# Performance work log

Measured on AMD Instinct MI355X. Metric: run time of the kernel, lower is better.

Reference implementation:

```python
import jax, jax.numpy as jnp
import numpy as np

W, B, S, D = 4, 1, 1024, 1024   # simulated world_size, batch, local seq, embed_dim
H, DS, HM = 16, 64, 4            # num_heads, summary_dim, meta_heads


def mha(q, k, v, w_in, b_in, w_out, b_out, nheads):
    """torch nn.MultiheadAttention (batch_first). Returns (out, head-averaged weights)."""
    d = q.shape[-1]
    hd = d // nheads
    wq, wk, wv = jnp.split(w_in, 3, axis=0)
    bq, bk, bv = jnp.split(b_in, 3)
    Bq, Sq, _ = q.shape
    Sk = k.shape[1]
    qh = (q @ wq.T + bq).reshape(Bq, Sq, nheads, hd)
    kh = (k @ wk.T + bk).reshape(Bq, Sk, nheads, hd)
    vh = (v @ wv.T + bv).reshape(Bq, Sk, nheads, hd)
    scores = jnp.einsum('bqhd,bkhd->bhqk', qh, kh) / float(np.sqrt(hd))
    attn = jax.nn.softmax(scores, axis=-1)
    out = jnp.einsum('bhqk,bkhd->bqhd', attn, vh).reshape(Bq, Sq, d)
    return out @ w_out.T + b_out, attn.mean(axis=1)


def attn_stats(attn):
    """attn: (B, S) -> (B, 4) [entropy, gini, max, top5]."""
    ent = -(attn * jnp.log(attn + 1e-8)).sum(-1, keepdims=True)
    s = jnp.sort(attn, axis=-1)
    n = attn.shape[-1]
    idx = jnp.arange(1, n + 1, dtype=attn.dtype)
    gini = 2.0 * (idx * s).sum(-1) / (n * s.sum(-1) + 1e-8) - (n + 1) / n
    mx = attn.max(-1, keepdims=True)
    k = min(5, n)
    top5 = jax.lax.top_k(attn, k)[0].sum(-1, keepdims=True)
    return jnp.concatenate([ent, gini[..., None], mx, top5], axis=-1)


def _forward(x, local_in_w, local_in_b, local_out_w, local_out_b,
             sum_query, sum_in_w, sum_in_b, sum_out_w, sum_out_b,
             pat_w1, pat_b1, pat_w2, pat_b2, comb_w, comb_b,
             meta_in_w, meta_in_b, meta_out_w, meta_out_b,
             route_w1, route_b1, route_w2, route_b2,
             cross_in_w, cross_in_b, cross_out_w, cross_out_b,
             gate_w, gate_b, proj_w, proj_b):
    nW = x.shape[0]

    # 1) local attention per rank: (W,B,S,D)
    local = jax.vmap(lambda xc: mha(xc, xc, xc, local_in_w, local_in_b,
                                    local_out_w, local_out_b, H)[0])(x)

    # 2) chunk summary per rank
    def summarize(lo):
        q = jnp.broadcast_to(sum_query, (lo.shape[0], 1, lo.shape[-1]))
        content, w = mha(q, lo, lo, sum_in_w, sum_in_b, sum_out_w, sum_out_b, H)
        content, w = content[:, 0], w[:, 0]              # (B,D), (B,S)
        pat = attn_stats(w)                               # (B,4)
        pat = jax.nn.relu(pat @ pat_w1.T + pat_b1) @ pat_w2.T + pat_b2
        return jnp.concatenate([content, pat], axis=-1) @ comb_w.T + comb_b

    summaries = jax.vmap(summarize)(local)                # (W,B,DS)
    all_sum = jnp.transpose(summaries, (1, 0, 2))         # (B,W,DS) = all-gather

    # 3) meta attention over chunk summaries -> routing weights
    refined, chunk_attn = mha(all_sum, all_sum, all_sum,
                              meta_in_w, meta_in_b, meta_out_w, meta_out_b, HM)
    logits = (jax.nn.relu(refined @ route_w1.T + route_b1) @ route_w2.T + route_b2)[..., 0]
    routing = jax.nn.softmax(logits, axis=-1)             # (B,W)

    all_chunks = jnp.transpose(local, (1, 0, 2, 3))       # (B,W,S,D) = all-gather

    # 4) selective cross-attention + gated combine, per rank
    def per_rank(r, lo):
        rm = routing * (1.0 - jax.nn.one_hot(r, nW, dtype=routing.dtype))
        rm = rm / (rm.sum(-1, keepdims=True) + 1e-8)
        kv = jnp.einsum('bw,bwsd->bsd', rm, all_chunks)
        cross, _ = mha(lo, kv, kv, cross_in_w, cross_in_b, cross_out_w, cross_out_b, H)
        g = jax.nn.sigmoid(jnp.concatenate([lo, cross], axis=-1) @ gate_w.T + gate_b)
        comb = g * cross + (1.0 - g) * lo
        return comb @ proj_w.T + proj_b

    out = jax.vmap(per_rank)(jnp.arange(nW), local)       # (W,B,S,D)
    return out


def setup_inputs() -> dict:
    key = jax.random.key(0)
    ks = iter(jax.random.split(key, 40))
    p = lambda *shape: jax.random.normal(next(ks), shape, dtype=jnp.float32) * 0.02
    inp = {
        'x': jax.random.normal(next(ks), (W, B, S, D), dtype=jnp.float32),
        'local_in_w': p(3 * D, D), 'local_in_b': p(3 * D),
        'local_out_w': p(D, D), 'local_out_b': p(D),
        'sum_query': p(1, 1, D),
        'sum_in_w': p(3 * D, D), 'sum_in_b': p(3 * D),
        'sum_out_w': p(D, D), 'sum_out_b': p(D),
        'pat_w1': p(DS, 4), 'pat_b1': p(DS),
        'pat_w2': p(DS, DS), 'pat_b2': p(DS),
        'comb_w': p(DS, D + DS), 'comb_b': p(DS),
        'meta_in_w': p(3 * DS, DS), 'meta_in_b': p(3 * DS),
        'meta_out_w': p(DS, DS), 'meta_out_b': p(DS),
        'route_w1': p(DS, DS), 'route_b1': p(DS),
        'route_w2': p(1, DS), 'route_b2': p(1),
        'cross_in_w': p(3 * D, D), 'cross_in_b': p(3 * D),
        'cross_out_w': p(D, D), 'cross_out_b': p(D),
        'gate_w': p(D, 2 * D), 'gate_b': p(D),
        'proj_w': p(D, D), 'proj_b': p(D),
    }
    return inp


def reference(x, local_in_w, local_in_b, local_out_w, local_out_b,
              sum_query, sum_in_w, sum_in_b, sum_out_w, sum_out_b,
              pat_w1, pat_b1, pat_w2, pat_b2, comb_w, comb_b,
              meta_in_w, meta_in_b, meta_out_w, meta_out_b,
              route_w1, route_b1, route_w2, route_b2,
              cross_in_w, cross_in_b, cross_out_w, cross_out_b,
              gate_w, gate_b, proj_w, proj_b):
    return _forward(x, local_in_w, local_in_b, local_out_w, local_out_b,
                    sum_query, sum_in_w, sum_in_b, sum_out_w, sum_out_b,
                    pat_w1, pat_b1, pat_w2, pat_b2, comb_w, comb_b,
                    meta_in_w, meta_in_b, meta_out_w, meta_out_b,
                    route_w1, route_b1, route_w2, route_b2,
                    cross_in_w, cross_in_b, cross_out_w, cross_out_b,
                    gate_w, gate_b, proj_w, proj_b)
```

## Files before the change

### kernel.cpp

```cpp
#include <hip/hip_runtime.h>
#include <hip/hip_bf16.h>
#include <stdint.h>

typedef uint16_t u16;
typedef __attribute__((ext_vector_type(8))) short short8;
typedef __attribute__((ext_vector_type(4))) short short4v;
typedef __attribute__((ext_vector_type(8))) unsigned short ushort8;
typedef __attribute__((ext_vector_type(4))) float f32x4;

#define AS1 __attribute__((address_space(1)))
#define AS3 __attribute__((address_space(3)))

__device__ __forceinline__ float b2f(u16 u){
  union{uint32_t i; float f;} v; v.i=((uint32_t)u)<<16; return v.f;
}
__device__ __forceinline__ u16 f2b(float f){
  union{uint32_t i; float f;} v; v.f=f;
  return (u16)((v.i + 0x7fffu + ((v.i>>16)&1u))>>16);
}
__device__ __forceinline__ u16 f2bf(float f){
  __hip_bfloat16 h = __float2bfloat16(f);
  return *reinterpret_cast<u16*>(&h);
}

struct CvtP { const float* src[8]; u16* dst[8]; long n[8]; };
__global__ void cvt_multi(CvtP p) {
  const int seg = blockIdx.y;
  const long i = ((long)blockIdx.x*256 + threadIdx.x)*8;
  if (i >= p.n[seg]) return;
  const float* in = p.src[seg];
  float4 a = *(const float4*)&in[i];
  float4 b = *(const float4*)&in[i+4];
  ushort8 o;
  o[0]=f2b(a.x); o[1]=f2b(a.y); o[2]=f2b(a.z); o[3]=f2b(a.w);
  o[4]=f2b(b.x); o[5]=f2b(b.y); o[6]=f2b(b.z); o[7]=f2b(b.w);
  *(ushort8*)&p.dst[seg][i] = o;
}

struct GemmP {
  const u16* A; const u16* B; u16* C; const float* bias;
  const u16* B2; u16* C2; const float* bias2;
  const u16* A2; const u16* lr; const u16* cr;
  long lda, ldb, ldc, ldb2, ldc2;
  int K, Nstore, Nstore2, ySplit, act, outf;
  float scale;
};

template<int BM>
__global__ __launch_bounds__(512) void gemm_nt(GemmP p) {
  constexpr int MI = BM / 32;
  __shared__ __align__(16) u16 lA[2][BM*32];
  __shared__ __align__(16) u16 lB[2][4096];
  const int t = threadIdx.x;
  const int wave = t >> 6, lane = t & 63;
  int by = blockIdx.y;
  const u16* Bp; u16* Cp; const float* bias; long ldb, ldc; int nst;
  if (by >= p.ySplit) {
    by -= p.ySplit; Bp = p.B2; Cp = p.C2; bias = p.bias2;
    ldb = p.ldb2; ldc = p.ldc2; nst = p.Nstore2;
  } else {
    Bp = p.B; Cp = p.C; bias = p.bias; ldb = p.ldb; ldc = p.ldc; nst = p.Nstore;
  }
  const u16* B = Bp + (long)by * 128 * ldb;
  const int srow = t >> 2, skk = (t & 3) * 8;
  const int wr = wave >> 2, wc = wave & 3;
  const int fr = lane & 15, fk = (lane >> 4) * 8;
  f32x4 acc[MI][2] = {};

  const int stepsPerSeg = p.K >> 5;
  const int nseg = p.A2 ? 2 : 1;
  const int total = nseg * stepsPerSeg;
  const u16* A0p = p.A + (long)blockIdx.x * BM * p.lda;
  const u16* A1p = p.A2 ? (p.A2 + (long)blockIdx.x * BM * p.lda) : A0p;

  auto stage = [&](int s, int b) {
    const int sg = (s >= stepsPerSeg) ? 1 : 0;
    const int k0 = (s - sg*stepsPerSeg) << 5;
    const u16* Ax = sg ? A1p : A0p;
    const u16* Bx = B + (long)sg * p.K;
    if (t < BM*4)
      __builtin_amdgcn_global_load_lds((const AS1 void*)(Ax + (long)srow*p.lda + k0 + skk),
                                       (AS3 void*)&lA[b][t*8], 16, 0, 0);
    __builtin_amdgcn_global_load_lds((const AS1 void*)(Bx + (long)srow*ldb + k0 + skk),
                                     (AS3 void*)&lB[b][t*8], 16, 0, 0);
  };

  stage(0, 0);
  __syncthreads();
  int cur = 0;
  for (int s = 0; s < total; ++s) {
    if (s + 1 < total) stage(s + 1, cur ^ 1);
    short8 av[MI], bv[2];
    #pragma unroll
    for (int mi = 0; mi < MI; ++mi) av[mi] = *(const short8*)&lA[cur][(wr*(BM/2) + mi*16 + fr)*32 + fk];
    #pragma unroll
    for (int ni = 0; ni < 2; ++ni) bv[ni] = *(const short8*)&lB[cur][(wc*32 + ni*16 + fr)*32 + fk];
    #pragma unroll
    for (int mi = 0; mi < MI; ++mi)
      #pragma unroll
      for (int ni = 0; ni < 2; ++ni)
        acc[mi][ni] = __builtin_amdgcn_mfma_f32_16x16x32_bf16(av[mi], bv[ni], acc[mi][ni], 0, 0, 0);
    __syncthreads();
    cur ^= 1;
  }

  const int rbase = blockIdx.x*BM + wr*(BM/2);
  const int cbase = by*128 + wc*32;
  const int rsub = (lane >> 4) * 4;
  #pragma unroll
  for (int ni = 0; ni < 2; ++ni) {
    const int col = cbase + ni*16 + fr;
    if (col >= nst) continue;
    const float bs = bias ? bias[col] : 0.f;
    #pragma unroll
    for (int mi = 0; mi < MI; ++mi) {
      #pragma unroll
      for (int j = 0; j < 4; ++j) {
        float v = acc[mi][ni][j] * p.scale + bs;
        const long idx = (long)(rbase + mi*16 + rsub + j) * ldc + col;
        if (p.act == 2) {
          const float gv = 1.f / (1.f + __expf(-v));
          const float cv = b2f(p.cr[idx]);
          const float lv = b2f(p.lr[idx]);
          Cp[idx] = f2b(gv*cv + (1.f - gv)*lv);
        } else {
          if (p.act == 1) v = 1.f / (1.f + __expf(-v));
          if (p.outf) ((float*)Cp)[idx] = v;
          else        Cp[idx] = f2b(v);
        }
      }
    }
  }
}

struct FlashP {
  const u16 *q, *k, *v; u16* o;
  long ldq, ldkv, ldo;
  long qB, kvB, oB;
};

__global__ __launch_bounds__(256) void flash_k(FlashP p) {
  const int t = threadIdx.x, w4 = t >> 6, lane = t & 63;
  const int bid = blockIdx.x;
  const int qt = bid >> 6;
  const int h  = bid & 15;
  const int wz = (bid >> 4) & 3;
  const int fr = lane & 15, g = lane >> 4, fk = g * 8;
  __shared__ __align__(16) u16 kt[64][72];
  __shared__ __align__(16) u16 vt[64][72];
  __shared__ __align__(16) u16 pl[4][32][72];

  const u16* Q = p.q + (long)wz*p.qB + (long)(qt*128 + w4*32)*p.ldq + h*64;
  const u16* K = p.k + (long)wz*p.kvB + h*64;
  const u16* V = p.v + (long)wz*p.kvB + h*64;

  short8 aq[2][2];
  #pragma unroll
  for (int f = 0; f < 2; ++f) {
    aq[f][0] = *(const short8*)&Q[(long)(f*16 + fr)*p.ldq + fk];
    aq[f][1] = *(const short8*)&Q[(long)(f*16 + fr)*p.ldq + 32 + fk];
  }

  f32x4 acc[2][4] = {};
  float ml[2] = {-3e38f, -3e38f}, ll[2] = {0.f, 0.f};
  const float C = 0.125f * 1.44269504f;

  const int krow = t >> 2, kseg = (t & 3) * 16;
  const int vp = t & 31, vc = (t >> 5) * 8;

  short8 kr0, kr1, vr0, vr1;
  kr0 = *(const short8*)&K[(long)krow*p.ldkv + kseg];
  kr1 = *(const short8*)&K[(long)krow*p.ldkv + kseg + 8];
  vr0 = *(const short8*)&V[(long)(2*vp)*p.ldkv + vc];
  vr1 = *(const short8*)&V[(long)(2*vp + 1)*p.ldkv + vc];

  for (int it = 0; it < 16; ++it) {
    *(short8*)&kt[krow][kseg]     = kr0;
    *(short8*)&kt[krow][kseg + 8] = kr1;
    #pragma unroll
    for (int e = 0; e < 8; ++e) {
      const uint32_t pk = (uint32_t)(uint16_t)vr0[e] | ((uint32_t)(uint16_t)vr1[e] << 16);
      *(uint32_t*)&vt[vc + e][2*vp] = pk;
    }
    __syncthreads();

    if (it + 1 < 16) {
      const int kn = (it + 1) * 64;
      kr0 = *(const short8*)&K[(long)(kn + krow)*p.ldkv + kseg];
      kr1 = *(const short8*)&K[(long)(kn + krow)*p.ldkv + kseg + 8];
      vr0 = *(const short8*)&V[(long)(kn + 2*vp)*p.ldkv + vc];
      vr1 = *(const short8*)&V[(long)(kn + 2*vp + 1)*p.ldkv + vc];
    }

    f32x4 s[2][4] = {};
    __builtin_amdgcn_s_setprio(1);
    #pragma unroll
    for (int ni = 0; ni < 4; ++ni) {
      short8 bk0 = *(const short8*)&kt[ni*16 + fr][fk];
      short8 bk1 = *(const short8*)&kt[ni*16 + fr][32 + fk];
      #pragma unroll
      for (int f = 0; f < 2; ++f) {
        s[f][ni] = __builtin_amdgcn_mfma_f32_16x16x32_bf16(bk0, aq[f][0], s[f][ni], 0, 0, 0);
        s[f][ni] = __builtin_amdgcn_mfma_f32_16x16x32_bf16(bk1, aq[f][1], s[f][ni], 0, 0, 0);
      }
    }
    __builtin_amdgcn_s_setprio(0);

    #pragma unroll
    for (int f = 0; f < 2; ++f) {
      float rm = s[f][0][0];
      #pragma unroll
      for (int ni = 0; ni < 4; ++ni)
        #pragma unroll
        for (int j = 0; j < 4; ++j) rm = fmaxf(rm, s[f][ni][j]);
      rm = fmaxf(rm, __shfl_xor(rm, 16, 64));
      rm = fmaxf(rm, __shfl_xor(rm, 32, 64));
      const float rml = rm * C;

      if (__any(rml > ml[f] + 11.5f)) {
        const float mnl = fmaxf(ml[f], rml);
        const float al = exp2f(ml[f] - mnl);
        const float a0 = __shfl(al, g*4 + 0, 64);
        const float a1 = __shfl(al, g*4 + 1, 64);
        const float a2 = __shfl(al, g*4 + 2, 64);
        const float a3 = __shfl(al, g*4 + 3, 64);
        #pragma unroll
        for (int nv = 0; nv < 4; ++nv) {
          acc[f][nv][0] *= a0; acc[f][nv][1] *= a1;
          acc[f][nv][2] *= a2; acc[f][nv][3] *= a3;
        }
        ll[f] *= al;
        ml[f] = mnl;
      }

      float rs = 0.f;
      u16 pb[4][4];
      #pragma unroll
      for (int ni = 0; ni < 4; ++ni)
        #pragma unroll
        for (int j = 0; j < 4; ++j) {
          const float pv = exp2f(s[f][ni][j]*C - ml[f]);
          rs += pv;
          pb[ni][j] = f2bf(pv);
        }
      rs += __shfl_xor(rs, 16, 64);
      rs += __shfl_xor(rs, 32, 64);
      ll[f] += rs;

      #pragma unroll
      for (int ni = 0; ni < 4; ++ni) {
        short4v pk4;
        pk4[0] = (short)pb[ni][0]; pk4[1] = (short)pb[ni][1];
        pk4[2] = (short)pb[ni][2]; pk4[3] = (short)pb[ni][3];
        *(short4v*)&pl[w4][f*16 + fr][ni*16 + g*4] = pk4;
      }
    }

    __builtin_amdgcn_s_setprio(1);
    #pragma unroll
    for (int ks = 0; ks < 2; ++ks) {
      short8 pa0 = *(const short8*)&pl[w4][fr][ks*32 + fk];
      short8 pa1 = *(const short8*)&pl[w4][16 + fr][ks*32 + fk];
      #pragma unroll
      for (int nv = 0; nv < 4; ++nv) {
        short8 bvv = *(const short8*)&vt[nv*16 + fr][ks*32 + fk];
        acc[0][nv] = __builtin_amdgcn_mfma_f32_16x16x32_bf16(pa0, bvv, acc[0][nv], 0, 0, 0);
        acc[1][nv] = __builtin_amdgcn_mfma_f32_16x16x32_bf16(pa1, bvv, acc[1][nv], 0, 0, 0);
      }
    }
    __builtin_amdgcn_s_setprio(0);
    __syncthreads();
  }

  u16* O = p.o + (long)wz*p.oB + (long)(qt*128 + w4*32)*p.ldo + h*64;
  #pragma unroll
  for (int f = 0; f < 2; ++f) {
    const float l0 = __shfl(ll[f], g*4 + 0, 64);
    const float l1 = __shfl(ll[f], g*4 + 1, 64);
    const float l2 = __shfl(ll[f], g*4 + 2, 64);
    const float l3 = __shfl(ll[f], g*4 + 3, 64);
    const float inv[4] = {1.f/l0, 1.f/l1, 1.f/l2, 1.f/l3};
    #pragma unroll
    for (int j = 0; j < 4; ++j)
      #pragma unroll
      for (int nv = 0; nv < 4; ++nv)
        O[(long)(f*16 + g*4 + j)*p.ldo + nv*16 + fr] = f2bf(acc[f][nv][j] * inv[j]);
  }
}

__global__ void gemv_qs(const float* sq, const float* w, const float* b, float* out) {
  const int t = threadIdx.x, nl = t & 63, kq = t >> 6;
  const int n = blockIdx.x*64 + nl;
  const float* row = w + (long)n * 1024 + kq*256;
  const float* q = sq + kq*256;
  float s = 0.f;
  for (int k = 0; k < 256; k += 4) {
    float4 ww = *(const float4*)&row[k];
    float4 qq = *(const float4*)&q[k];
    s += qq.x*ww.x + qq.y*ww.y + qq.z*ww.z + qq.w*ww.w;
  }
  __shared__ float ps[4][64];
  ps[kq][nl] = s;
  __syncthreads();
  if (t < 64) out[blockIdx.x*64 + t] = ps[0][t]+ps[1][t]+ps[2][t]+ps[3][t] + b[blockIdx.x*64 + t];
}

__global__ void sum_attend(const float* qs, const u16* sumkv, float* content, float* pall) {
  const int h = blockIdx.x, w = blockIdx.y, t = threadIdx.x;
  const int lane = t & 63, wv = t >> 6;
  __shared__ float qsh[64];
  __shared__ float sc[1024];
  __shared__ float rmax[4], rsum[4];
  __shared__ float po[4][64];
  if (t < 64) qsh[t] = qs[h*64 + t];
  __syncthreads();
  const u16* kbase = sumkv + (long)w*2097152 + h*64;
  float e[4];
  float mx = -1e30f;
  #pragma unroll
  for (int j = 0; j < 4; ++j) {
    const int k = j*256 + t;
    const u16* krow = kbase + (long)k * 2048;
    float s = 0.f;
    #pragma unroll
    for (int d = 0; d < 64; d += 8) {
      ushort8 kk = *(const ushort8*)&krow[d];
      #pragma unroll
      for (int q = 0; q < 8; ++q) s += qsh[d+q] * b2f(kk[q]);
    }
    s *= 0.125f;
    e[j] = s;
    mx = fmaxf(mx, s);
  }
  #pragma unroll
  for (int o = 32; o; o >>= 1) mx = fmaxf(mx, __shfl_xor(mx, o, 64));
  if (lane == 0) rmax[wv] = mx;
  __syncthreads();
  mx = fmaxf(fmaxf(rmax[0],rmax[1]), fmaxf(rmax[2],rmax[3]));
  float sum = 0.f;
  #pragma unroll
  for (int j = 0; j < 4; ++j) { e[j] = __expf(e[j]-mx); sum += e[j]; }
  #pragma unroll
  for (int o = 32; o; o >>= 1) sum += __shfl_xor(sum, o, 64);
  if (lane == 0) rsum[wv] = sum;
  __syncthreads();
  const float inv = 1.f / (rsum[0]+rsum[1]+rsum[2]+rsum[3]);
  float* pr = pall + ((long)w*16 + h)*1024;
  #pragma unroll
  for (int j = 0; j < 4; ++j) {
    const int k = j*256 + t;
    const float pn = e[j]*inv;
    sc[k] = pn;
    pr[k] = pn;
  }
  __syncthreads();
  const u16* vbase = sumkv + (long)w*2097152 + 1024 + h*64;
  float o = 0.f;
  const int k0 = wv*256;
  for (int k = k0; k < k0+256; ++k) o += sc[k] * b2f(vbase[(long)k*2048 + lane]);
  po[wv][lane] = o;
  __syncthreads();
  if (t < 64) content[(long)w*1024 + h*64 + t] = po[0][t]+po[1][t]+po[2][t]+po[3][t];
}

__global__ void wavg_k(const float* pall, float* wavg) {
  const int w = blockIdx.y, k = blockIdx.x*256 + threadIdx.x;
  float s = 0.f;
  #pragma unroll
  for (int h = 0; h < 16; ++h) s += pall[((long)w*16 + h)*1024 + k];
  wavg[w*1024 + k] = s * (1.f/16.f);
}

__global__ void contproj_k(const float* content, const float* w_, const float* b, float* out) {
  const int w = blockIdx.y, t = threadIdx.x;
  const int nl = t & 63, kq = t >> 6;
  const int n = blockIdx.x*64 + nl;
  const float* c = content + w*1024 + kq*256;
  const float* row = w_ + (long)n * 1024 + kq*256;
  float s = 0.f;
  for (int k = 0; k < 256; k += 4) {
    float4 ww = *(const float4*)&row[k];
    s += c[k]*ww.x + c[k+1]*ww.y + c[k+2]*ww.z + c[k+3]*ww.w;
  }
  __shared__ float ps[4][64];
  ps[kq][nl] = s;
  __syncthreads();
  if (t < 64) out[w*1024 + blockIdx.x*64 + t] = ps[0][t]+ps[1][t]+ps[2][t]+ps[3][t] + b[blockIdx.x*64 + t];
}

__global__ void stats1_k(const float* wavg, float* part) {
  const int c = blockIdx.x, w = blockIdx.y, t = threadIdx.x;
  __shared__ float a[1024];
  for (int i = t; i < 1024; i += 256) a[i] = wavg[w*1024 + i];
  __syncthreads();
  const int jl = t & 63, iq = t >> 6;
  const int j = c*64 + jl;
  const float aj = a[j];
  int pr = 0;
  const int i0 = iq*256;
  #pragma unroll 8
  for (int i = i0; i < i0+256; ++i) {
    const float ai = a[i];
    pr += (ai < aj) || (ai == aj && i < j);
  }
  __shared__ int prs[4][64];
  prs[iq][jl] = pr;
  __syncthreads();
  if (t < 64) {
    const int rank = 1 + prs[0][jl] + prs[1][jl] + prs[2][jl] + prs[3][jl];
    float ent = -aj * logf(aj + 1e-8f);
    float gnum = (float)rank * aj;
    float ssum = aj;
    float mx = aj;
    float top5 = (rank >= 1020) ? aj : 0.f;
    #pragma unroll
    for (int o = 32; o; o >>= 1) {
      ent += __shfl_xor(ent, o, 64);
      gnum += __shfl_xor(gnum, o, 64);
      ssum += __shfl_xor(ssum, o, 64);
      mx = fmaxf(mx, __shfl_xor(mx, o, 64));
      top5 += __shfl_xor(top5, o, 64);
    }
    if (t == 0) {
      float* pp = part + ((w*16 + c) * 5);
      pp[0]=ent; pp[1]=gnum; pp[2]=ssum; pp[3]=mx; pp[4]=top5;
    }
  }
}

__global__ void stats2_k(const float* part, float* stats) {
  const int w = blockIdx.x, t = threadIdx.x;
  const int c = t & 15, stat = t >> 4;
  float v = 0.f;
  const bool active = stat < 5;
  if (active) v = part[(w*16 + c)*5 + stat];
  #pragma unroll
  for (int o = 8; o; o >>= 1) {
    const float ov = __shfl_xor(v, o, 64);
    v = (stat == 3) ? fmaxf(v, ov) : (v + ov);
  }
  __shared__ float r5[5];
  if (active && c == 0) r5[stat] = v;
  __syncthreads();
  if (t == 0) {
    stats[w*4+0] = r5[0];
    stats[w*4+1] = 2.f*r5[1]/(1024.f*r5[2] + 1e-8f) - 1025.f/1024.f;
    stats[w*4+2] = r5[3];
    stats[w*4+3] = r5[4];
  }
}

__global__ void patsum_k(const float* stats, const float* contprj,
                         const float* pw1, const float* pb1, const float* pw2, const float* pb2,
                         const float* combw, const float* combb, float* summ) {
  const int w = blockIdx.x, t = threadIdx.x;
  const int nl = t & 63, kq = t >> 6;
  __shared__ float p1[64], pat[64];
  __shared__ float ps[4][64];
  __shared__ float ps2[4][64];
  if (t < 64) {
    float s = 0.f;
    #pragma unroll
    for (int k = 0; k < 4; ++k) s += stats[w*4+k] * pw1[t*4+k];
    p1[t] = fmaxf(s + pb1[t], 0.f);
  }
  __syncthreads();
  {
    float s = 0.f;
    const float* rw = pw2 + (long)nl*64 + kq*16;
    const float* pp = p1 + kq*16;
    #pragma unroll
    for (int k = 0; k < 16; ++k) s += pp[k] * rw[k];
    ps[kq][nl] = s;
  }
  __syncthreads();
  if (t < 64) pat[t] = ps[0][t]+ps[1][t]+ps[2][t]+ps[3][t] + pb2[t];
  __syncthreads();
  const float* c = contprj + w*1024;
  const float* row = combw + (long)nl * 1088;
  float s = 0.f;
  const int k0 = kq*272;
  for (int k = k0; k < k0+272; ++k) {
    const float rv = row[k];
    const float cv = (k < 1024) ? c[k] : pat[k-1024];
    s += cv * rv;
  }
  ps2[kq][nl] = s;
  __syncthreads();
  if (t < 64) summ[w*64 + t] = ps2[0][t]+ps2[1][t]+ps2[2][t]+ps2[3][t] + combb[t];
}

__global__ void meta_k(const float* summ, const float* miw, const float* mib,
                       const float* mow, const float* mob, const float* rw1, const float* rb1,
                       const float* rw2, const float* rb2, float* routing) {
  const int t = threadIdx.x;
  __shared__ float qkv[4][192];
  __shared__ float sc[64];
  __shared__ float o[4][64];
  __shared__ float rf[4][64];
  __shared__ float t1[4][64];
  __shared__ float lg[4];
  for (int idx = t; idx < 768; idx += 64) {
    const int w = idx / 192, rrow = idx % 192;
    const float* rw = miw + (long)rrow * 64;
    float s = 0.f;
    for (int k = 0; k < 64; ++k) s += summ[w*64+k] * rw[k];
    qkv[w][rrow] = s + mib[rrow];
  }
  __syncthreads();
  {
    const int h = t >> 4, i = (t >> 2) & 3, j = t & 3;
    float s = 0.f;
    #pragma unroll
    for (int d = 0; d < 16; ++d) s += qkv[i][h*16+d] * qkv[j][64 + h*16+d];
    sc[t] = s * 0.25f;
  }
  __syncthreads();
  if (t < 16) {
    const float a0=sc[t*4], a1=sc[t*4+1], a2=sc[t*4+2], a3=sc[t*4+3];
    const float m = fmaxf(fmaxf(a0,a1), fmaxf(a2,a3));
    const float e0=__expf(a0-m), e1=__expf(a1-m), e2=__expf(a2-m), e3=__expf(a3-m);
    const float s = e0+e1+e2+e3;
    sc[t*4]=e0/s; sc[t*4+1]=e1/s; sc[t*4+2]=e2/s; sc[t*4+3]=e3/s;
  }
  __syncthreads();
  for (int idx = t; idx < 256; idx += 64) {
    const int i = idx >> 6, c = idx & 63, h = c >> 4;
    float s = 0.f;
    #pragma unroll
    for (int j = 0; j < 4; ++j) s += sc[(h*4+i)*4+j] * qkv[j][128 + c];
    o[i][c] = s;
  }
  __syncthreads();
  for (int idx = t; idx < 256; idx += 64) {
    const int i = idx >> 6, n = idx & 63;
    const float* rw = mow + (long)n * 64;
    float s = 0.f;
    for (int k = 0; k < 64; ++k) s += o[i][k] * rw[k];
    rf[i][n] = s + mob[n];
  }
  __syncthreads();
  for (int idx = t; idx < 256; idx += 64) {
    const int i = idx >> 6, n = idx & 63;
    const float* rw = rw1 + (long)n * 64;
    float s = 0.f;
    for (int k = 0; k < 64; ++k) s += rf[i][k] * rw[k];
    t1[i][n] = fmaxf(s + rb1[n], 0.f);
  }
  __syncthreads();
  if (t < 4) {
    float s = 0.f;
    for (int k = 0; k < 64; ++k) s += t1[t][k] * rw2[k];
    lg[t] = s + rb2[0];
  }
  __syncthreads();
  if (t == 0) {
    const float m = fmaxf(fmaxf(lg[0],lg[1]), fmaxf(lg[2],lg[3]));
    float e[4], s = 0.f;
    #pragma unroll
    for (int i = 0; i < 4; ++i) { e[i] = __expf(lg[i]-m); s += e[i]; }
    #pragma unroll
    for (int i = 0; i < 4; ++i) routing[i] = e[i]/s;
  }
}

__global__ void kvr_k(const u16* local, const float* routing, u16* kvr) {
  const int r = blockIdx.y;
  const long e = ((long)blockIdx.x*256 + threadIdx.x) * 8;
  float rm[4]; float s = 0.f;
  #pragma unroll
  for (int w = 0; w < 4; ++w) { rm[w] = (w == r) ? 0.f : routing[w]; s += rm[w]; }
  const float inv = 1.f / (s + 1e-8f);
  ushort8 a0 = *(const ushort8*)&local[e];
  ushort8 a1 = *(const ushort8*)&local[1048576 + e];
  ushort8 a2 = *(const ushort8*)&local[2097152 + e];
  ushort8 a3 = *(const ushort8*)&local[3145728 + e];
  ushort8 out;
  #pragma unroll
  for (int j = 0; j < 8; ++j)
    out[j] = f2b((rm[0]*b2f(a0[j]) + rm[1]*b2f(a1[j]) + rm[2]*b2f(a2[j]) + rm[3]*b2f(a3[j])) * inv);
  *(ushort8*)&kvr[(long)r*1048576 + e] = out;
}

template<int BM>
static void gemmT(hipStream_t st, dim3 grid,
                  const u16* A, long lda, const u16* B, long ldb,
                  u16* C, long ldc, const float* bias,
                  int K, int N, float scale, int act, int outf) {
  GemmP p = {};
  p.A=A; p.B=B; p.C=C; p.bias=bias;
  p.lda=lda; p.ldb=ldb; p.ldc=ldc;
  p.K=K; p.Nstore=N; p.ySplit=1<<30; p.act=act; p.outf=outf; p.scale=scale;
  gemm_nt<BM><<<grid, dim3(512), 0, st>>>(p);
}

extern "C" void kernel_launch(void* const* d_in, const int* in_sizes, int n_in,
                              void* d_out, int out_size, void* d_ws, size_t ws_size,
                              hipStream_t stream) {
  (void)in_sizes; (void)n_in; (void)out_size; (void)ws_size;
  const float* x   = (const float*)d_in[0];
  const float* liw = (const float*)d_in[1];
  const float* lib = (const float*)d_in[2];
  const float* low = (const float*)d_in[3];
  const float* lob = (const float*)d_in[4];
  const float* sq  = (const float*)d_in[5];
  const float* siw = (const float*)d_in[6];
  const float* sib = (const float*)d_in[7];
  const float* sow = (const float*)d_in[8];
  const float* sob = (const float*)d_in[9];
  const float* pw1 = (const float*)d_in[10];
  const float* pb1 = (const float*)d_in[11];
  const float* pw2 = (const float*)d_in[12];
  const float* pb2 = (const float*)d_in[13];
  const float* cbw = (const float*)d_in[14];
  const float* cbb = (const float*)d_in[15];
  const float* miw = (const float*)d_in[16];
  const float* mib = (const float*)d_in[17];
  const float* mow = (const float*)d_in[18];
  const float* mob = (const float*)d_in[19];
  const float* rw1 = (const float*)d_in[20];
  const float* rb1 = (const float*)d_in[21];
  const float* rw2 = (const float*)d_in[22];
  const float* rb2 = (const float*)d_in[23];
  const float* ciw = (const float*)d_in[24];
  const float* cib = (const float*)d_in[25];
  const float* cow = (const float*)d_in[26];
  const float* cob = (const float*)d_in[27];
  const float* gw  = (const float*)d_in[28];
  const float* gb  = (const float*)d_in[29];
  const float* pw  = (const float*)d_in[30];
  const float* pb  = (const float*)d_in[31];

  char* ws = (char*)d_ws;
  u16* qkv    = (u16*)(ws + 0);
  u16* aout   = (u16*)(ws + 25165824);
  u16* local  = (u16*)(ws + 33554432);
  u16* scratch= (u16*)(ws + 41943040);
  u16* s2048  = (u16*)(ws + 79691776);
  u16* cq     = (u16*)(ws + 96468992);
  u16* kvr    = (u16*)(ws + 104857600);
  u16* crossb = (u16*)(ws + 113246208);
  char* sf = ws + 121634816;
  float* qs      = (float*)(sf + 0);
  float* pall    = (float*)(sf + 4096);
  float* wavg    = (float*)(sf + 266240);
  float* content = (float*)(sf + 282624);
  float* contprj = (float*)(sf + 299008);
  float* stats   = (float*)(sf + 315392);
  float* summ    = (float*)(sf + 315456);
  float* routing = (float*)(sf + 316480);
  float* part    = (float*)(sf + 316544);
  u16* siwkvb = (u16*)(ws + 122028032);
  u16* lowb   = (u16*)(ws + 126222336);
  u16* ciwb   = (u16*)(ws + 128319488);
  u16* cowb   = (u16*)(ws + 134610944);
  u16* gwb    = (u16*)(ws + 136708096);
  u16* pwb    = (u16*)(ws + 140902400);
  u16* xb   = crossb;
  u16* liwb = scratch;

  CvtP cp;
  cp.src[0]=x;   cp.dst[0]=xb;     cp.n[0]=4194304;
  cp.src[1]=liw; cp.dst[1]=liwb;   cp.n[1]=3145728;
  cp.src[2]=low; cp.dst[2]=lowb;   cp.n[2]=1048576;
  cp.src[3]=siw+1048576; cp.dst[3]=siwkvb; cp.n[3]=2097152;
  cp.src[4]=ciw; cp.dst[4]=ciwb;   cp.n[4]=3145728;
  cp.src[5]=cow; cp.dst[5]=cowb;   cp.n[5]=1048576;
  cp.src[6]=gw;  cp.dst[6]=gwb;    cp.n[6]=2097152;
  cp.src[7]=pw;  cp.dst[7]=pwb;    cp.n[7]=1048576;
  cvt_multi<<<dim3(2048, 8), dim3(256), 0, stream>>>(cp);

  gemmT<128>(stream, dim3(32,24), xb,1024, liwb,1024, qkv,3072, lib, 1024, 3072, 1.f, 0, 0);

  {
    FlashP fp;
    fp.q = qkv; fp.k = qkv + 1024; fp.v = qkv + 2048; fp.o = aout;
    fp.ldq = 3072; fp.ldkv = 3072; fp.ldo = 1024;
    fp.qB = 3145728; fp.kvB = 3145728; fp.oB = 1048576;
    flash_k<<<dim3(512), dim3(256), 0, stream>>>(fp);
  }

  gemmT<64>(stream, dim3(64,8), aout,1024, lowb,1024, local,1024, lob, 1024, 1024, 1.f, 0, 0);

  {
    GemmP p = {};
    p.A = local; p.lda = 1024; p.K = 1024; p.scale = 1.f;
    p.B = ciwb;   p.C = cq;    p.bias = cib;      p.ldb = 1024; p.ldc = 1024; p.Nstore = 1024;
    p.B2 = siwkvb; p.C2 = s2048; p.bias2 = sib+1024; p.ldb2 = 1024; p.ldc2 = 2048; p.Nstore2 = 2048;
    p.ySplit = 8;
    gemm_nt<128><<<dim3(32,24), dim3(512), 0, stream>>>(p);
  }

  gemv_qs<<<dim3(16), dim3(256), 0, stream>>>(sq, siw, sib, qs);
  sum_attend<<<dim3(16,4), dim3(256), 0, stream>>>(qs, s2048, content, pall);
  wavg_k<<<dim3(4,4), dim3(256), 0, stream>>>(pall, wavg);
  contproj_k<<<dim3(16,4), dim3(256), 0, stream>>>(content, sow, sob, contprj);
  stats1_k<<<dim3(16,4), dim3(256), 0, stream>>>(wavg, part);
  stats2_k<<<dim3(4), dim3(128), 0, stream>>>(part, stats);
  patsum_k<<<dim3(4), dim3(256), 0, stream>>>(stats, contprj, pw1, pb1, pw2, pb2, cbw, cbb, summ);

  meta_k<<<dim3(1), dim3(64), 0, stream>>>(summ, miw, mib, mow, mob, rw1, rb1, rw2, rb2, routing);

  kvr_k<<<dim3(512,4), dim3(256), 0, stream>>>(local, routing, kvr);

  gemmT<128>(stream, dim3(32,16), kvr,1024, ciwb+1048576,1024, s2048,2048, cib+1024, 1024, 2048, 1.f, 0, 0);

  {
    FlashP fp;
    fp.q = cq; fp.k = s2048; fp.v = s2048 + 1024; fp.o = aout;
    fp.ldq = 1024; fp.ldkv = 2048; fp.ldo = 1024;
    fp.qB = 1048576; fp.kvB = 2097152; fp.oB = 1048576;
    flash_k<<<dim3(512), dim3(256), 0, stream>>>(fp);
  }

  gemmT<64>(stream, dim3(64,8), aout,1024, cowb,1024, crossb,1024, cob, 1024, 1024, 1.f, 0, 0);

  {
    GemmP p = {};
    p.A = local; p.A2 = crossb; p.lr = local; p.cr = crossb;
    p.B = gwb; p.C = kvr; p.bias = gb;
    p.lda = 1024; p.ldb = 2048; p.ldc = 1024;
    p.K = 1024; p.Nstore = 1024; p.ySplit = 1<<30; p.act = 2; p.outf = 0; p.scale = 1.f;
    gemm_nt<64><<<dim3(64,8), dim3(512), 0, stream>>>(p);
  }

  gemmT<64>(stream, dim3(64,8), kvr,1024, pwb,1024, (u16*)d_out,1024, pb, 1024, 1024, 1.f, 0, 1);
}
```

Baseline: 425.5 us.

## Split flash attention over two KV halves and merge partials

Each flash attention launch now splits the key/value sequence into two halves, doubling the grid from 512 to 1024 blocks. Each half writes unnormalized fp32 partial outputs plus running max and sum to workspace. A new merge kernel rescales and combines the two partials into the bf16 output. The aim is better occupancy on a GPU with many CUs, at the cost of extra fp32 global traffic and one more launch per attention.

```diff
diff --git a/kernel.cpp b/kernel.cpp
--- a/kernel.cpp
+++ b/kernel.cpp
@@ -135,6 +135,7 @@
 
 struct FlashP {
   const u16 *q, *k, *v; u16* o;
+  float* pO; float* pml;
   long ldq, ldkv, ldo;
   long qB, kvB, oB;
 };
@@ -142,17 +143,19 @@
 __global__ __launch_bounds__(256) void flash_k(FlashP p) {
   const int t = threadIdx.x, w4 = t >> 6, lane = t & 63;
   const int bid = blockIdx.x;
-  const int qt = bid >> 6;
-  const int h  = bid & 15;
-  const int wz = (bid >> 4) & 3;
+  const int half = bid >> 9;
+  const int sub = bid & 511;
+  const int qt = sub >> 6;
+  const int h  = sub & 15;
+  const int wz = (sub >> 4) & 3;
   const int fr = lane & 15, g = lane >> 4, fk = g * 8;
   __shared__ __align__(16) u16 kt[64][72];
   __shared__ __align__(16) u16 vt[64][72];
   __shared__ __align__(16) u16 pl[4][32][72];
 
   const u16* Q = p.q + (long)wz*p.qB + (long)(qt*128 + w4*32)*p.ldq + h*64;
-  const u16* K = p.k + (long)wz*p.kvB + h*64;
-  const u16* V = p.v + (long)wz*p.kvB + h*64;
+  const u16* K = p.k + (long)wz*p.kvB + h*64 + (long)(half*512)*p.ldkv;
+  const u16* V = p.v + (long)wz*p.kvB + h*64 + (long)(half*512)*p.ldkv;
 
   short8 aq[2][2];
   #pragma unroll
@@ -174,7 +177,7 @@
   vr0 = *(const short8*)&V[(long)(2*vp)*p.ldkv + vc];
   vr1 = *(const short8*)&V[(long)(2*vp + 1)*p.ldkv + vc];
 
-  for (int it = 0; it < 16; ++it) {
+  for (int it = 0; it < 8; ++it) {
     *(short8*)&kt[krow][kseg]     = kr0;
     *(short8*)&kt[krow][kseg + 8] = kr1;
     #pragma unroll
@@ -184,7 +187,7 @@
     }
     __syncthreads();
 
-    if (it + 1 < 16) {
+    if (it + 1 < 8) {
       const int kn = (it + 1) * 64;
       kr0 = *(const short8*)&K[(long)(kn + krow)*p.ldkv + kseg];
       kr1 = *(const short8*)&K[(long)(kn + krow)*p.ldkv + kseg + 8];
@@ -272,19 +275,46 @@
     __syncthreads();
   }
 
-  u16* O = p.o + (long)wz*p.oB + (long)(qt*128 + w4*32)*p.ldo + h*64;
+  const long Rbase = ((long)(wz*16 + h))*1024 + qt*128 + w4*32;
+  float* PO  = p.pO  + (long)half*65536*64;
+  float* PML = p.pml + (long)half*65536*2;
   #pragma unroll
   for (int f = 0; f < 2; ++f) {
-    const float l0 = __shfl(ll[f], g*4 + 0, 64);
-    const float l1 = __shfl(ll[f], g*4 + 1, 64);
-    const float l2 = __shfl(ll[f], g*4 + 2, 64);
-    const float l3 = __shfl(ll[f], g*4 + 3, 64);
-    const float inv[4] = {1.f/l0, 1.f/l1, 1.f/l2, 1.f/l3};
     #pragma unroll
     for (int j = 0; j < 4; ++j)
       #pragma unroll
       for (int nv = 0; nv < 4; ++nv)
-        O[(long)(f*16 + g*4 + j)*p.ldo + nv*16 + fr] = f2bf(acc[f][nv][j] * inv[j]);
+        PO[(Rbase + f*16 + g*4 + j)*64 + nv*16 + fr] = acc[f][nv][j];
+    if (g == 0) {
+      PML[(Rbase + f*16 + fr)*2    ] = ml[f];
+      PML[(Rbase + f*16 + fr)*2 + 1] = ll[f];
+    }
+  }
+}
+
+__global__ __launch_bounds__(256) void fmerge_k(const float* pO, const float* pml, u16* out) {
+  const int t = threadIdx.x;
+  const long r = (long)blockIdx.x*64 + (t >> 2);
+  const int dq = (t & 3) * 16;
+  const float m0 = pml[r*2],            l0 = pml[r*2 + 1];
+  const float m1 = pml[131072 + r*2],   l1 = pml[131072 + r*2 + 1];
+  const float m  = fmaxf(m0, m1);
+  const float a0 = exp2f(m0 - m), a1 = exp2f(m1 - m);
+  const float inv = 1.f / (l0*a0 + l1*a1);
+  const float s0 = a0*inv, s1 = a1*inv;
+  const long  o0 = r*64 + dq;
+  const long  o1 = 4194304L + r*64 + dq;
+  const int wz = (int)(r >> 14), rem = (int)(r & 16383);
+  const int h = rem >> 10, qrow = rem & 1023;
+  u16* ob = out + (long)wz*1048576 + (long)qrow*1024 + h*64 + dq;
+  #pragma unroll
+  for (int dd = 0; dd < 4; ++dd) {
+    float4 v0 = *(const float4*)&pO[o0 + dd*4];
+    float4 v1 = *(const float4*)&pO[o1 + dd*4];
+    ob[dd*4 + 0] = f2bf(v0.x*s0 + v1.x*s1);
+    ob[dd*4 + 1] = f2bf(v0.y*s0 + v1.y*s1);
+    ob[dd*4 + 2] = f2bf(v0.z*s0 + v1.z*s1);
+    ob[dd*4 + 3] = f2bf(v0.w*s0 + v1.w*s1);
   }
 }
 
@@ -658,6 +688,8 @@
   u16* pwb    = (u16*)(ws + 140902400);
   u16* xb   = crossb;
   u16* liwb = scratch;
+  float* pO  = (float*)(ws + 41943040);
+  float* pml = (float*)(ws + 41943040 + 33554432);
 
   CvtP cp;
   cp.src[0]=x;   cp.dst[0]=xb;     cp.n[0]=4194304;
@@ -675,9 +707,11 @@
   {
     FlashP fp;
     fp.q = qkv; fp.k = qkv + 1024; fp.v = qkv + 2048; fp.o = aout;
+    fp.pO = pO; fp.pml = pml;
     fp.ldq = 3072; fp.ldkv = 3072; fp.ldo = 1024;
     fp.qB = 3145728; fp.kvB = 3145728; fp.oB = 1048576;
-    flash_k<<<dim3(512), dim3(256), 0, stream>>>(fp);
+    flash_k<<<dim3(1024), dim3(256), 0, stream>>>(fp);
+    fmerge_k<<<dim3(1024), dim3(256), 0, stream>>>(pO, pml, aout);
   }
 
   gemmT<64>(stream, dim3(64,8), aout,1024, lowb,1024, local,1024, lob, 1024, 1024, 1.f, 0, 0);
@@ -708,9 +742,11 @@
   {
     FlashP fp;
     fp.q = cq; fp.k = s2048; fp.v = s2048 + 1024; fp.o = aout;
+    fp.pO = pO; fp.pml = pml;
     fp.ldq = 1024; fp.ldkv = 2048; fp.ldo = 1024;
     fp.qB = 1048576; fp.kvB = 2097152; fp.oB = 1048576;
-    flash_k<<<dim3(512), dim3(256), 0, stream>>>(fp);
+    flash_k<<<dim3(1024), dim3(256), 0, stream>>>(fp);
+    fmerge_k<<<dim3(1024), dim3(256), 0, stream>>>(pO, pml, aout);
   }
 
   gemmT<64>(stream, dim3(64,8), aout,1024, cowb,1024, crossb,1024, cob, 1024, 1024, 1.f, 0, 0);
```

Result: slower. 462.7 us (+8.7%).
